# Kernel optimization log

Measured on AMD Instinct MI355X. Metric: run time of the kernel, lower is better.

Reference implementation:

```python
import jax, jax.numpy as jnp
import numpy as np

N_HEADS = 16
THETA = 10000.0


def _rope_cos_sin(seq_len, head_dim):
    # freqs_cis = exp(i * pos * theta^(-2j/d)), shape (seq_len, head_dim//2)
    inv_freq = 1.0 / (THETA ** (np.arange(0, head_dim, 2, dtype=np.float32) / head_dim))
    ang = np.arange(seq_len, dtype=np.float32)[:, None] * inv_freq[None, :]
    return jnp.asarray(np.cos(ang)), jnp.asarray(np.sin(ang))


def _apply_rope(t, cos, sin):
    # t: [B, S, H, hd]; rotate consecutive pairs as complex numbers
    B, S, H, hd = t.shape
    pairs = t.reshape(B, S, H, hd // 2, 2)
    r, i = pairs[..., 0], pairs[..., 1]
    c = cos[None, :, None, :]  # [1, S, 1, hd//2]
    s = sin[None, :, None, :]
    out_r = r * c - i * s
    out_i = r * s + i * c
    return jnp.stack([out_r, out_i], axis=-1).reshape(B, S, H, hd)


def setup_inputs() -> dict:
    key = jax.random.key(0)
    ks = jax.random.split(key, 5)
    B, S, D = 2, 2048, 2048
    scale = 1.0 / np.sqrt(D)
    return {
        "x": jax.random.normal(ks[0], (B, S, D), dtype=jnp.float32),
        "wq": jax.random.normal(ks[1], (D, D), dtype=jnp.float32) * scale,
        "wk": jax.random.normal(ks[2], (D, D), dtype=jnp.float32) * scale,
        "wv": jax.random.normal(ks[3], (D, D), dtype=jnp.float32) * scale,
        "wo": jax.random.normal(ks[4], (D, D), dtype=jnp.float32) * scale,
    }


def reference(x, wq, wk, wv, wo):
    B, S, D = x.shape
    H = N_HEADS
    hd = D // H
    cos, sin = _rope_cos_sin(S, hd)

    xq = (x @ wq.T).reshape(B, S, H, hd)
    xk = (x @ wk.T).reshape(B, S, H, hd)
    xv = (x @ wv.T).reshape(B, S, H, hd)

    xq = _apply_rope(xq, cos, sin)
    xk = _apply_rope(xk, cos, sin)

    # [B, H, S, S] scores, full (non-causal) softmax as in the source
    scores = jnp.einsum("bqhd,bkhd->bhqk", xq, xk) / jnp.sqrt(jnp.float32(hd))
    attn = jax.nn.softmax(scores, axis=-1)
    out = jnp.einsum("bhqk,bkhd->bqhd", attn, xv).reshape(B, S, D)
    return out @ wo.T
```

## Files before the change

### kernel.cpp

```cpp
#include <hip/hip_runtime.h>
#include <hip/hip_bf16.h>
#include <stdint.h>


typedef __attribute__((ext_vector_type(4))) float f32x4;
typedef __attribute__((ext_vector_type(8))) short bf16x8;

typedef __attribute__((address_space(3))) unsigned int lds_u32;
typedef __attribute__((address_space(1))) const unsigned int gbl_u32;

__device__ __forceinline__ void async16(const void* g, void* l) {
  __builtin_amdgcn_global_load_lds((gbl_u32*)g, (lds_u32*)l, 16, 0, 0);
}

__device__ __forceinline__ float bf_to_f(unsigned short u) {
  union { unsigned int i; float f; } v; v.i = ((unsigned int)u) << 16; return v.f;
}
__device__ __forceinline__ unsigned short f_to_bf(float f) {
  union { float f; unsigned int i; } v; v.f = f;
  unsigned int r = v.i + 0x7FFFu + ((v.i >> 16) & 1u);
  return (unsigned short)(r >> 16);
}
__device__ __forceinline__ unsigned int cvt_pk_bf16(float lo, float hi) {
  unsigned int r;
  asm("v_cvt_pk_bf16_f32 %0, %1, %2" : "=v"(r) : "v"(lo), "v"(hi));
  return r;
}

#define B_ 2
#define S_ 2048
#define D_ 2048
#define H_ 16
#define HD_ 128
#define KVB 128

__global__ __launch_bounds__(256) void conv_all(const float* __restrict__ x,
                                                const float* __restrict__ wq,
                                                const float* __restrict__ wk,
                                                const float* __restrict__ wv,
                                                const float* __restrict__ wo,
                                                unsigned short* __restrict__ xb,
                                                unsigned short* __restrict__ wb) {
  int i = blockIdx.x * 256 + threadIdx.x;
  const float* s;
  unsigned short* d;
  int off;
  if (i < 2097152) {
    s = x; d = xb; off = i;
  } else {
    int j = i - 2097152;
    int t = j >> 20;
    off = j & 1048575;
    s = (t == 0) ? wq : (t == 1) ? wk : (t == 2) ? wv : wo;
    d = wb + (size_t)t * 4194304;
  }
  float4 v = ((const float4*)s)[off];
  uint2 o;
  o.x = (unsigned int)f_to_bf(v.x) | ((unsigned int)f_to_bf(v.y) << 16);
  o.y = (unsigned int)f_to_bf(v.z) | ((unsigned int)f_to_bf(v.w) << 16);
  ((uint2*)d)[off] = o;
}

__global__ __launch_bounds__(256) void rope_table_kernel(float* __restrict__ cosT,
                                                         float* __restrict__ sinT) {
  int i = blockIdx.x * 256 + threadIdx.x;
  int s = i >> 6, j = i & 63;
  float inv = powf(10000.0f, -(float)(2 * j) * (1.0f / 128.0f));
  float ang = (float)s * inv;
  float sv, cv;
  sincosf(ang, &sv, &cv);
  cosT[i] = cv;
  sinT[i] = sv;
}

__global__ __launch_bounds__(256, 3) void qkv_gemm(const unsigned short* __restrict__ A,
                                                   const unsigned short* __restrict__ W,
                                                   unsigned short* __restrict__ Qb,
                                                   unsigned short* __restrict__ Kb,
                                                   unsigned short* __restrict__ Vtb,
                                                   const float* __restrict__ cosT,
                                                   const float* __restrict__ sinT) {
  __shared__ unsigned short sA[128 * 64];
  __shared__ unsigned short sB[128 * 64];
  const int K = 2048, N = 2048;
  const int tid = threadIdx.x;
  const int l = tid & 63, wv = tid >> 6;
  const int lane15 = l & 15, lhi = l >> 4;
  const int wm = wv >> 1, wn = wv & 1;
  const int bm = blockIdx.x, bn = blockIdx.y;
  const int sector = bn >> 4, bnl = bn & 15;
  const unsigned short* Ag = A + (size_t)bm * 128 * K;
  const unsigned short* Bg = W + (size_t)bn * 128 * K;

  f32x4 acc[4][4];
  const f32x4 zero = {0.f, 0.f, 0.f, 0.f};
#pragma unroll
  for (int i = 0; i < 4; i++)
#pragma unroll
    for (int j = 0; j < 4; j++) acc[i][j] = zero;

  for (int k0 = 0; k0 < K; k0 += 64) {
    __syncthreads();
#pragma unroll
    for (int i = 0; i < 4; i++) {
      int c = i * 256 + tid;
      int row = c >> 3;
      int colD = (c & 7) << 4;
      int colS = colD ^ ((row & 7) << 4);
      async16(Ag + (size_t)row * K + k0 + (colS >> 1), (char*)sA + row * 128 + colD);
      async16(Bg + (size_t)row * K + k0 + (colS >> 1), (char*)sB + row * 128 + colD);
    }
    __syncthreads();

#pragma unroll
    for (int h = 0; h < 2; h++) {
      bf16x8 af[4], bfr[4];
#pragma unroll
      for (int i = 0; i < 4; i++) {
        int row = wm * 64 + i * 16 + lane15;
        af[i] = *(const bf16x8*)((char*)sA + row * 128 +
                                 ((h * 64 + lhi * 16) ^ ((row & 7) << 4)));
      }
#pragma unroll
      for (int j = 0; j < 4; j++) {
        int row = wn * 64 + j * 16 + lane15;
        bfr[j] = *(const bf16x8*)((char*)sB + row * 128 +
                                  ((h * 64 + lhi * 16) ^ ((row & 7) << 4)));
      }
#pragma unroll
      for (int i = 0; i < 4; i++)
#pragma unroll
        for (int j = 0; j < 4; j++)
          acc[i][j] = __builtin_amdgcn_mfma_f32_16x16x32_bf16(af[i], bfr[j], acc[i][j], 0, 0, 0);
    }
  }

#pragma unroll
  for (int i = 0; i < 4; i++) {
    int m0 = bm * 128 + wm * 64 + i * 16 + lhi * 4;
#pragma unroll
    for (int j = 0; j < 4; j++) {
      int n = bnl * 128 + wn * 64 + j * 16 + lane15;
      if (sector == 0) {
#pragma unroll
        for (int r = 0; r < 4; r++) Qb[(size_t)(m0 + r) * N + n] = f_to_bf(acc[i][j][r]);
      } else if (sector == 1) {
        int s0 = m0 & (S_ - 1);
        int jp = (n & (HD_ - 1)) >> 1;
        int odd = n & 1;
#pragma unroll
        for (int r = 0; r < 4; r++) {
          float own = acc[i][j][r];
          float prt = __shfl_xor(own, 1);
          float c = cosT[(s0 + r) * 64 + jp];
          float sn = sinT[(s0 + r) * 64 + jp];
          float outv = odd ? fmaf(prt, sn, own * c) : own * c - prt * sn;
          Kb[(size_t)(m0 + r) * N + n] = f_to_bf(outv);
        }
      } else {
        int s0 = m0 & (S_ - 1);
        size_t row = (size_t)((m0 >> 11) * D_ + n);
        uint2 st;
        st.x = (unsigned int)f_to_bf(acc[i][j][0]) | ((unsigned int)f_to_bf(acc[i][j][1]) << 16);
        st.y = (unsigned int)f_to_bf(acc[i][j][2]) | ((unsigned int)f_to_bf(acc[i][j][3]) << 16);
        *(uint2*)(Vtb + row * S_ + s0) = st;
      }
    }
  }
}

__global__ __launch_bounds__(256, 3) void gemm_out(const unsigned short* __restrict__ A,
                                                   const unsigned short* __restrict__ Bm,
                                                   float* __restrict__ Cf) {
  __shared__ unsigned short sA[128 * 64];
  __shared__ unsigned short sB[128 * 64];
  const int K = 2048, N = 2048;
  const int tid = threadIdx.x;
  const int l = tid & 63, wv = tid >> 6;
  const int lane15 = l & 15, lhi = l >> 4;
  const int wm = wv >> 1, wn = wv & 1;
  const int bm = blockIdx.x, bn = blockIdx.y;
  const unsigned short* Ag = A + (size_t)bm * 128 * K;
  const unsigned short* Bg = Bm + (size_t)bn * 128 * K;

  f32x4 acc[4][4];
  const f32x4 zero = {0.f, 0.f, 0.f, 0.f};
#pragma unroll
  for (int i = 0; i < 4; i++)
#pragma unroll
    for (int j = 0; j < 4; j++) acc[i][j] = zero;

  for (int k0 = 0; k0 < K; k0 += 64) {
    __syncthreads();
#pragma unroll
    for (int i = 0; i < 4; i++) {
      int c = i * 256 + tid;
      int row = c >> 3;
      int colD = (c & 7) << 4;
      int colS = colD ^ ((row & 7) << 4);
      async16(Ag + (size_t)row * K + k0 + (colS >> 1), (char*)sA + row * 128 + colD);
      async16(Bg + (size_t)row * K + k0 + (colS >> 1), (char*)sB + row * 128 + colD);
    }
    __syncthreads();

#pragma unroll
    for (int h = 0; h < 2; h++) {
      bf16x8 af[4], bfr[4];
#pragma unroll
      for (int i = 0; i < 4; i++) {
        int row = wm * 64 + i * 16 + lane15;
        af[i] = *(const bf16x8*)((char*)sA + row * 128 +
                                 ((h * 64 + lhi * 16) ^ ((row & 7) << 4)));
      }
#pragma unroll
      for (int j = 0; j < 4; j++) {
        int row = wn * 64 + j * 16 + lane15;
        bfr[j] = *(const bf16x8*)((char*)sB + row * 128 +
                                  ((h * 64 + lhi * 16) ^ ((row & 7) << 4)));
      }
#pragma unroll
      for (int i = 0; i < 4; i++)
#pragma unroll
        for (int j = 0; j < 4; j++)
          acc[i][j] = __builtin_amdgcn_mfma_f32_16x16x32_bf16(af[i], bfr[j], acc[i][j], 0, 0, 0);
    }
  }

#pragma unroll
  for (int i = 0; i < 4; i++) {
    int m0 = bm * 128 + wm * 64 + i * 16 + lhi * 4;
#pragma unroll
    for (int j = 0; j < 4; j++) {
      int n = bn * 128 + wn * 64 + j * 16 + lane15;
#pragma unroll
      for (int r = 0; r < 4; r++) Cf[(size_t)(m0 + r) * N + n] = acc[i][j][r];
    }
  }
}

__global__ __launch_bounds__(512, 2) void attn_kernel(const unsigned short* __restrict__ Q,
                                                      const unsigned short* __restrict__ K,
                                                      const unsigned short* __restrict__ Vt,
                                                      unsigned short* __restrict__ ctx,
                                                      const float* __restrict__ cosT,
                                                      const float* __restrict__ sinT) {
  __shared__ unsigned short sK[2][KVB * 128];
  __shared__ unsigned short sV[2][128 * KVB];
  const int tid = threadIdx.x, l = tid & 63, w = tid >> 6;
  const int lane15 = l & 15, lhi = l >> 4;
  const int bh = blockIdx.x * 4 + (blockIdx.y >> 3);
  const int qt = blockIdx.y & 7;
  const int b = bh >> 4, h = bh & 15;
  const int q0 = qt * 256;
  const unsigned short* Kg = K + ((size_t)(b * S_)) * D_ + h * HD_;
  const unsigned short* Vg = Vt + ((size_t)bh * HD_) * S_;
  const float qscale = 0.08838834764831845f * 1.44269504f;
  const float THR = 11.5415603f;

  const unsigned short* gp[8];
  unsigned int lofs[8];
  size_t gstep;
  if (w < 4) {
#pragma unroll
    for (int i = 0; i < 8; i++) {
      int row = w * 32 + i * 4 + (l >> 4);
      int colD = (l & 15) << 4;
      int colS = colD ^ ((row & 7) << 4);
      gp[i] = Kg + (size_t)row * D_ + (colS >> 1);
      lofs[i] = row * 256 + colD;
    }
    gstep = (size_t)KVB * D_;
  } else {
#pragma unroll
    for (int i = 0; i < 8; i++) {
      int row = (w - 4) * 32 + i * 4 + (l >> 4);
      int colD = (l & 15) << 4;
      int colS = colD ^ ((row & 7) << 4);
      gp[i] = Vg + (size_t)row * S_ + (colS >> 1);
      lofs[i] = row * 256 + colD;
    }
    gstep = KVB;
  }

  bf16x8 qf[2][4];
#pragma unroll
  for (int s = 0; s < 2; s++) {
    int s_q = q0 + w * 32 + s * 16 + lane15;
    const unsigned short* Qrow = Q + ((size_t)(b * S_ + s_q)) * D_ + h * HD_;
#pragma unroll
    for (int kc = 0; kc < 4; kc++) {
      int d0 = kc * 32 + lhi * 8;
      uint4 raw = *(const uint4*)(Qrow + d0);
      float4 cv = *(const float4*)(cosT + (size_t)s_q * 64 + (d0 >> 1));
      float4 sv = *(const float4*)(sinT + (size_t)s_q * 64 + (d0 >> 1));
      unsigned int u[4] = {raw.x, raw.y, raw.z, raw.w};
      float cc[4] = {cv.x, cv.y, cv.z, cv.w};
      float ss[4] = {sv.x, sv.y, sv.z, sv.w};
      unsigned int o[4];
#pragma unroll
      for (int p = 0; p < 4; p++) {
        float re = bf_to_f((unsigned short)(u[p] & 0xffffu));
        float im = bf_to_f((unsigned short)(u[p] >> 16));
        float orr = (re * cc[p] - im * ss[p]) * qscale;
        float oi = (re * ss[p] + im * cc[p]) * qscale;
        o[p] = (unsigned int)f_to_bf(orr) | ((unsigned int)f_to_bf(oi) << 16);
      }
      union { uint4 u4; bf16x8 v; } cvt;
      cvt.u4.x = o[0]; cvt.u4.y = o[1]; cvt.u4.z = o[2]; cvt.u4.w = o[3];
      qf[s][kc] = cvt.v;
    }
  }

  float mrun[2] = {-1e30f, -1e30f}, lrun[2] = {0.f, 0.f};
  const f32x4 zero = {0.f, 0.f, 0.f, 0.f};
  f32x4 oacc[2][8];
#pragma unroll
  for (int s = 0; s < 2; s++)
#pragma unroll
    for (int nf = 0; nf < 8; nf++) oacc[s][nf] = zero;

  {
    char* base = (w < 4) ? (char*)&sK[0][0] : (char*)&sV[0][0];
#pragma unroll
    for (int i = 0; i < 8; i++) { async16(gp[i], base + lofs[i]); gp[i] += gstep; }
  }

  for (int t = 0; t < S_ / KVB; ++t) {
    const int cur = t & 1;
    __syncthreads();
    if (t < S_ / KVB - 1) {
      char* base = (w < 4) ? (char*)&sK[cur ^ 1][0] : (char*)&sV[cur ^ 1][0];
#pragma unroll
      for (int i = 0; i < 8; i++) { async16(gp[i], base + lofs[i]); gp[i] += gstep; }
    }
    const unsigned short* sKc = sK[cur];
    const unsigned short* sVc = sV[cur];

    f32x4 sacc[2][8];
#pragma unroll
    for (int s = 0; s < 2; s++)
#pragma unroll
      for (int n = 0; n < 8; n++) sacc[s][n] = zero;
    __builtin_amdgcn_s_setprio(1);
#pragma unroll
    for (int n = 0; n < 8; n++) {
      int row = n * 16 + lane15;
#pragma unroll
      for (int kc = 0; kc < 4; kc++) {
        bf16x8 kf = *(const bf16x8*)((const char*)sKc + row * 256 +
                                     ((kc * 64 + lhi * 16) ^ ((row & 7) << 4)));
        sacc[0][n] = __builtin_amdgcn_mfma_f32_16x16x32_bf16(kf, qf[0][kc], sacc[0][n], 0, 0, 0);
        sacc[1][n] = __builtin_amdgcn_mfma_f32_16x16x32_bf16(kf, qf[1][kc], sacc[1][n], 0, 0, 0);
      }
    }
    __builtin_amdgcn_s_setprio(0);

    float pmax[2];
#pragma unroll
    for (int s = 0; s < 2; s++) {
      float mn[8];
#pragma unroll
      for (int n = 0; n < 8; n++)
        mn[n] = fmaxf(fmaxf(sacc[s][n][0], sacc[s][n][1]), fmaxf(sacc[s][n][2], sacc[s][n][3]));
      float pm = fmaxf(fmaxf(fmaxf(mn[0], mn[1]), fmaxf(mn[2], mn[3])),
                       fmaxf(fmaxf(mn[4], mn[5]), fmaxf(mn[6], mn[7])));
      pm = fmaxf(pm, __shfl_xor(pm, 16));
      pm = fmaxf(pm, __shfl_xor(pm, 32));
      pmax[s] = pm;
    }
    if (!__all(fmaxf(pmax[0] - mrun[0], pmax[1] - mrun[1]) <= THR)) {
#pragma unroll
      for (int s = 0; s < 2; s++) {
        float mnew = fmaxf(mrun[s], pmax[s]);
        float alpha = exp2f(mrun[s] - mnew);
        lrun[s] *= alpha;
        float af[4];
#pragma unroll
        for (int r = 0; r < 4; r++) af[r] = __shfl(alpha, lhi * 4 + r);
#pragma unroll
        for (int nf = 0; nf < 8; nf++)
#pragma unroll
          for (int r = 0; r < 4; r++) oacc[s][nf][r] *= af[r];
        mrun[s] = mnew;
      }
    }
    bf16x8 paS[2][4];
#pragma unroll
    for (int s = 0; s < 2; s++) {
      float rs = 0.f;
      unsigned int wlo[8], whi[8];
#pragma unroll
      for (int n = 0; n < 8; n++) {
        float p0 = exp2f(sacc[s][n][0] - mrun[s]);
        float p1 = exp2f(sacc[s][n][1] - mrun[s]);
        float p2 = exp2f(sacc[s][n][2] - mrun[s]);
        float p3 = exp2f(sacc[s][n][3] - mrun[s]);
        rs += (p0 + p1) + (p2 + p3);
        wlo[n] = cvt_pk_bf16(p0, p1);
        whi[n] = cvt_pk_bf16(p2, p3);
      }
      rs += __shfl_xor(rs, 16);
      rs += __shfl_xor(rs, 32);
      lrun[s] += rs;
#pragma unroll
      for (int kc = 0; kc < 4; kc++) {
        unsigned int A = wlo[2 * kc], Bw = whi[2 * kc];
        unsigned int C = wlo[2 * kc + 1], Dw = whi[2 * kc + 1];
        asm("v_permlane32_swap_b32 %0, %1" : "+v"(A), "+v"(C));
        asm("v_permlane16_swap_b32 %0, %1" : "+v"(A), "+v"(C));
        asm("v_permlane32_swap_b32 %0, %1" : "+v"(Bw), "+v"(Dw));
        asm("v_permlane16_swap_b32 %0, %1" : "+v"(Bw), "+v"(Dw));
        union { uint4 u4; bf16x8 v; } pk;
        pk.u4.x = A; pk.u4.y = Bw; pk.u4.z = C; pk.u4.w = Dw;
        paS[s][kc] = pk.v;
      }
    }

    __builtin_amdgcn_s_setprio(1);
#pragma unroll
    for (int nf = 0; nf < 8; nf++) {
      int row = nf * 16 + lane15;
#pragma unroll
      for (int kc = 0; kc < 4; kc++) {
        bf16x8 vf = *(const bf16x8*)((const char*)sVc + row * 256 +
                                     ((kc * 64 + lhi * 16) ^ ((row & 7) << 4)));
        oacc[0][nf] = __builtin_amdgcn_mfma_f32_16x16x32_bf16(paS[0][kc], vf, oacc[0][nf], 0, 0, 0);
        oacc[1][nf] = __builtin_amdgcn_mfma_f32_16x16x32_bf16(paS[1][kc], vf, oacc[1][nf], 0, 0, 0);
      }
    }
    __builtin_amdgcn_s_setprio(0);
  }

#pragma unroll
  for (int s = 0; s < 2; s++) {
    float inv = 1.0f / lrun[s];
    float invr[4];
#pragma unroll
    for (int r = 0; r < 4; r++) invr[r] = __shfl(inv, lhi * 4 + r);
    unsigned short* Og = ctx + ((size_t)(b * S_ + q0 + w * 32 + s * 16)) * D_ + h * HD_;
#pragma unroll
    for (int r = 0; r < 4; r++) {
      int qrow = lhi * 4 + r;
#pragma unroll
      for (int nf = 0; nf < 8; nf++)
        Og[(size_t)qrow * D_ + nf * 16 + lane15] = f_to_bf(oacc[s][nf][r] * invr[r]);
    }
  }
}

extern "C" void kernel_launch(void* const* d_in, const int* in_sizes, int n_in,
                              void* d_out, int out_size, void* d_ws, size_t ws_size,
                              hipStream_t stream) {
  (void)in_sizes; (void)n_in; (void)out_size; (void)ws_size;
  const float* x = (const float*)d_in[0];
  const float* wq = (const float*)d_in[1];
  const float* wk = (const float*)d_in[2];
  const float* wv = (const float*)d_in[3];
  const float* wo = (const float*)d_in[4];
  float* out = (float*)d_out;

  char* ws = (char*)d_ws;
  const size_t MB = 1024 * 1024;
  unsigned short* xb  = (unsigned short*)(ws + 0 * MB);
  unsigned short* wqb = (unsigned short*)(ws + 16 * MB);
  unsigned short* wob = (unsigned short*)(ws + 40 * MB);
  unsigned short* Qb  = (unsigned short*)(ws + 48 * MB);
  unsigned short* Kb  = (unsigned short*)(ws + 64 * MB);
  unsigned short* Vtb = (unsigned short*)(ws + 80 * MB);
  float* cosT = (float*)(ws + 96 * MB);
  float* sinT = (float*)(ws + 96 * MB + 524288);
  unsigned short* ctxb = xb;

  const int M = B_ * S_;

  conv_all<<<24576, 256, 0, stream>>>(x, wq, wk, wv, wo, xb, wqb);
  rope_table_kernel<<<512, 256, 0, stream>>>(cosT, sinT);

  qkv_gemm<<<dim3(M / 128, 48), 256, 0, stream>>>(xb, wqb, Qb, Kb, Vtb, cosT, sinT);

  attn_kernel<<<dim3(8, 32), 512, 0, stream>>>(Qb, Kb, Vtb, ctxb, cosT, sinT);

  gemm_out<<<dim3(M / 128, D_ / 128), 256, 0, stream>>>(ctxb, wob, out);
}
```

Measured before the change: 272.0 us.

## Double-buffer LDS tiles in QKV and output GEMMs with MFMA priority boost

Both GEMM kernels now keep two LDS stages for the A and B tiles. The next K-slice is prefetched with async global-to-LDS loads while MFMAs run on the current slice, and each iteration needs one barrier instead of two. Source pointers and LDS offsets are precomputed and advanced each step. s_setprio is raised around the MFMA block. The cost is twice the LDS per block, so launch bounds drop from 3 to 2 blocks per CU, which lowers occupancy in exchange for overlapping load latency with compute.

```diff
diff --git a/kernel.cpp b/kernel.cpp
--- a/kernel.cpp
+++ b/kernel.cpp
@@ -73,15 +73,15 @@
   sinT[i] = sv;
 }
 
-__global__ __launch_bounds__(256, 3) void qkv_gemm(const unsigned short* __restrict__ A,
+__global__ __launch_bounds__(256, 2) void qkv_gemm(const unsigned short* __restrict__ A,
                                                    const unsigned short* __restrict__ W,
                                                    unsigned short* __restrict__ Qb,
                                                    unsigned short* __restrict__ Kb,
                                                    unsigned short* __restrict__ Vtb,
                                                    const float* __restrict__ cosT,
                                                    const float* __restrict__ sinT) {
-  __shared__ unsigned short sA[128 * 64];
-  __shared__ unsigned short sB[128 * 64];
+  __shared__ unsigned short sA[2][128 * 64];
+  __shared__ unsigned short sB[2][128 * 64];
   const int K = 2048, N = 2048;
   const int tid = threadIdx.x;
   const int l = tid & 63, wv = tid >> 6;
@@ -89,8 +89,20 @@
   const int wm = wv >> 1, wn = wv & 1;
   const int bm = blockIdx.x, bn = blockIdx.y;
   const int sector = bn >> 4, bnl = bn & 15;
-  const unsigned short* Ag = A + (size_t)bm * 128 * K;
-  const unsigned short* Bg = W + (size_t)bn * 128 * K;
+
+  const int srow = tid >> 3;
+  const int colD = (tid & 7) << 4;
+  const unsigned short* aSrc[4];
+  const unsigned short* bSrc[4];
+  unsigned int lofs[4];
+#pragma unroll
+  for (int i = 0; i < 4; i++) {
+    int row = i * 32 + srow;
+    int cS = colD ^ ((row & 7) << 4);
+    aSrc[i] = A + (size_t)(bm * 128 + row) * K + (cS >> 1);
+    bSrc[i] = W + (size_t)(bn * 128 + row) * K + (cS >> 1);
+    lofs[i] = row * 128 + colD;
+  }
 
   f32x4 acc[4][4];
   const f32x4 zero = {0.f, 0.f, 0.f, 0.f};
@@ -99,18 +111,24 @@
 #pragma unroll
     for (int j = 0; j < 4; j++) acc[i][j] = zero;
 
-  for (int k0 = 0; k0 < K; k0 += 64) {
+#pragma unroll
+  for (int i = 0; i < 4; i++) {
+    async16(aSrc[i], (char*)&sA[0][0] + lofs[i]); aSrc[i] += 64;
+    async16(bSrc[i], (char*)&sB[0][0] + lofs[i]); bSrc[i] += 64;
+  }
+
+  for (int t = 0; t < 32; ++t) {
+    const int cur = t & 1;
     __syncthreads();
-#pragma unroll
-    for (int i = 0; i < 4; i++) {
-      int c = i * 256 + tid;
-      int row = c >> 3;
-      int colD = (c & 7) << 4;
-      int colS = colD ^ ((row & 7) << 4);
-      async16(Ag + (size_t)row * K + k0 + (colS >> 1), (char*)sA + row * 128 + colD);
-      async16(Bg + (size_t)row * K + k0 + (colS >> 1), (char*)sB + row * 128 + colD);
-    }
-    __syncthreads();
+    if (t < 31) {
+#pragma unroll
+      for (int i = 0; i < 4; i++) {
+        async16(aSrc[i], (char*)&sA[cur ^ 1][0] + lofs[i]); aSrc[i] += 64;
+        async16(bSrc[i], (char*)&sB[cur ^ 1][0] + lofs[i]); bSrc[i] += 64;
+      }
+    }
+    const char* sAc = (const char*)&sA[cur][0];
+    const char* sBc = (const char*)&sB[cur][0];
 
 #pragma unroll
     for (int h = 0; h < 2; h++) {
@@ -118,20 +136,22 @@
 #pragma unroll
       for (int i = 0; i < 4; i++) {
         int row = wm * 64 + i * 16 + lane15;
-        af[i] = *(const bf16x8*)((char*)sA + row * 128 +
+        af[i] = *(const bf16x8*)(sAc + row * 128 +
                                  ((h * 64 + lhi * 16) ^ ((row & 7) << 4)));
       }
 #pragma unroll
       for (int j = 0; j < 4; j++) {
         int row = wn * 64 + j * 16 + lane15;
-        bfr[j] = *(const bf16x8*)((char*)sB + row * 128 +
+        bfr[j] = *(const bf16x8*)(sBc + row * 128 +
                                   ((h * 64 + lhi * 16) ^ ((row & 7) << 4)));
       }
+      __builtin_amdgcn_s_setprio(1);
 #pragma unroll
       for (int i = 0; i < 4; i++)
 #pragma unroll
         for (int j = 0; j < 4; j++)
           acc[i][j] = __builtin_amdgcn_mfma_f32_16x16x32_bf16(af[i], bfr[j], acc[i][j], 0, 0, 0);
+      __builtin_amdgcn_s_setprio(0);
     }
   }
 
@@ -169,19 +189,31 @@
   }
 }
 
-__global__ __launch_bounds__(256, 3) void gemm_out(const unsigned short* __restrict__ A,
+__global__ __launch_bounds__(256, 2) void gemm_out(const unsigned short* __restrict__ A,
                                                    const unsigned short* __restrict__ Bm,
                                                    float* __restrict__ Cf) {
-  __shared__ unsigned short sA[128 * 64];
-  __shared__ unsigned short sB[128 * 64];
+  __shared__ unsigned short sA[2][128 * 64];
+  __shared__ unsigned short sB[2][128 * 64];
   const int K = 2048, N = 2048;
   const int tid = threadIdx.x;
   const int l = tid & 63, wv = tid >> 6;
   const int lane15 = l & 15, lhi = l >> 4;
   const int wm = wv >> 1, wn = wv & 1;
   const int bm = blockIdx.x, bn = blockIdx.y;
-  const unsigned short* Ag = A + (size_t)bm * 128 * K;
-  const unsigned short* Bg = Bm + (size_t)bn * 128 * K;
+
+  const int srow = tid >> 3;
+  const int colD = (tid & 7) << 4;
+  const unsigned short* aSrc[4];
+  const unsigned short* bSrc[4];
+  unsigned int lofs[4];
+#pragma unroll
+  for (int i = 0; i < 4; i++) {
+    int row = i * 32 + srow;
+    int cS = colD ^ ((row & 7) << 4);
+    aSrc[i] = A + (size_t)(bm * 128 + row) * K + (cS >> 1);
+    bSrc[i] = Bm + (size_t)(bn * 128 + row) * K + (cS >> 1);
+    lofs[i] = row * 128 + colD;
+  }
 
   f32x4 acc[4][4];
   const f32x4 zero = {0.f, 0.f, 0.f, 0.f};
@@ -190,18 +222,24 @@
 #pragma unroll
     for (int j = 0; j < 4; j++) acc[i][j] = zero;
 
-  for (int k0 = 0; k0 < K; k0 += 64) {
+#pragma unroll
+  for (int i = 0; i < 4; i++) {
+    async16(aSrc[i], (char*)&sA[0][0] + lofs[i]); aSrc[i] += 64;
+    async16(bSrc[i], (char*)&sB[0][0] + lofs[i]); bSrc[i] += 64;
+  }
+
+  for (int t = 0; t < 32; ++t) {
+    const int cur = t & 1;
     __syncthreads();
-#pragma unroll
-    for (int i = 0; i < 4; i++) {
-      int c = i * 256 + tid;
-      int row = c >> 3;
-      int colD = (c & 7) << 4;
-      int colS = colD ^ ((row & 7) << 4);
-      async16(Ag + (size_t)row * K + k0 + (colS >> 1), (char*)sA + row * 128 + colD);
-      async16(Bg + (size_t)row * K + k0 + (colS >> 1), (char*)sB + row * 128 + colD);
-    }
-    __syncthreads();
+    if (t < 31) {
+#pragma unroll
+      for (int i = 0; i < 4; i++) {
+        async16(aSrc[i], (char*)&sA[cur ^ 1][0] + lofs[i]); aSrc[i] += 64;
+        async16(bSrc[i], (char*)&sB[cur ^ 1][0] + lofs[i]); bSrc[i] += 64;
+      }
+    }
+    const char* sAc = (const char*)&sA[cur][0];
+    const char* sBc = (const char*)&sB[cur][0];
 
 #pragma unroll
     for (int h = 0; h < 2; h++) {
@@ -209,20 +247,22 @@
 #pragma unroll
       for (int i = 0; i < 4; i++) {
         int row = wm * 64 + i * 16 + lane15;
-        af[i] = *(const bf16x8*)((char*)sA + row * 128 +
+        af[i] = *(const bf16x8*)(sAc + row * 128 +
                                  ((h * 64 + lhi * 16) ^ ((row & 7) << 4)));
       }
 #pragma unroll
       for (int j = 0; j < 4; j++) {
         int row = wn * 64 + j * 16 + lane15;
-        bfr[j] = *(const bf16x8*)((char*)sB + row * 128 +
+        bfr[j] = *(const bf16x8*)(sBc + row * 128 +
                                   ((h * 64 + lhi * 16) ^ ((row & 7) << 4)));
       }
+      __builtin_amdgcn_s_setprio(1);
 #pragma unroll
       for (int i = 0; i < 4; i++)
 #pragma unroll
         for (int j = 0; j < 4; j++)
           acc[i][j] = __builtin_amdgcn_mfma_f32_16x16x32_bf16(af[i], bfr[j], acc[i][j], 0, 0, 0);
+      __builtin_amdgcn_s_setprio(0);
     }
   }
 
```

Result: no change. 267.5 us (-1.7%).

## Double-buffer LDS tiles in QKV and output GEMMs with async prefetch

Applied to the files above, without the earlier changes.

Both projection GEMMs now split each K step into 32-wide tiles held in two LDS buffers. The async global-to-LDS load for the next tile is issued right after the single barrier, so it overlaps the MFMA work on the current tile. This removes the old second barrier per step, which stalled on load completion before any compute could start. Source pointers and LDS offsets are precomputed with a new swizzle, and s_setprio raises wave priority around the MFMA block. In exchange there are twice as many loop iterations and barriers per K, and a smaller tile per step.

```diff
diff --git a/kernel.cpp b/kernel.cpp
--- a/kernel.cpp
+++ b/kernel.cpp
@@ -80,8 +80,8 @@
                                                    unsigned short* __restrict__ Vtb,
                                                    const float* __restrict__ cosT,
                                                    const float* __restrict__ sinT) {
-  __shared__ unsigned short sA[128 * 64];
-  __shared__ unsigned short sB[128 * 64];
+  __shared__ unsigned short sA[2][128 * 32];
+  __shared__ unsigned short sB[2][128 * 32];
   const int K = 2048, N = 2048;
   const int tid = threadIdx.x;
   const int l = tid & 63, wv = tid >> 6;
@@ -89,8 +89,20 @@
   const int wm = wv >> 1, wn = wv & 1;
   const int bm = blockIdx.x, bn = blockIdx.y;
   const int sector = bn >> 4, bnl = bn & 15;
-  const unsigned short* Ag = A + (size_t)bm * 128 * K;
-  const unsigned short* Bg = W + (size_t)bn * 128 * K;
+
+  const unsigned short* aSrc[2];
+  const unsigned short* bSrc[2];
+  unsigned int lofs[2];
+#pragma unroll
+  for (int i = 0; i < 2; i++) {
+    int c = i * 256 + tid;
+    int row = c >> 2;
+    int colD = (c & 3) << 4;
+    int colS = colD ^ (((row >> 1) & 3) << 4);
+    aSrc[i] = A + (size_t)(bm * 128 + row) * K + (colS >> 1);
+    bSrc[i] = W + (size_t)(bn * 128 + row) * K + (colS >> 1);
+    lofs[i] = row * 64 + colD;
+  }
 
   f32x4 acc[4][4];
   const f32x4 zero = {0.f, 0.f, 0.f, 0.f};
@@ -99,40 +111,45 @@
 #pragma unroll
     for (int j = 0; j < 4; j++) acc[i][j] = zero;
 
-  for (int k0 = 0; k0 < K; k0 += 64) {
+#pragma unroll
+  for (int i = 0; i < 2; i++) {
+    async16(aSrc[i], (char*)&sA[0][0] + lofs[i]); aSrc[i] += 32;
+    async16(bSrc[i], (char*)&sB[0][0] + lofs[i]); bSrc[i] += 32;
+  }
+
+  for (int t = 0; t < 64; ++t) {
+    const int cur = t & 1;
     __syncthreads();
+    if (t < 63) {
+#pragma unroll
+      for (int i = 0; i < 2; i++) {
+        async16(aSrc[i], (char*)&sA[cur ^ 1][0] + lofs[i]); aSrc[i] += 32;
+        async16(bSrc[i], (char*)&sB[cur ^ 1][0] + lofs[i]); bSrc[i] += 32;
+      }
+    }
+    const char* sAc = (const char*)&sA[cur][0];
+    const char* sBc = (const char*)&sB[cur][0];
+
+    bf16x8 af[4], bfr[4];
 #pragma unroll
     for (int i = 0; i < 4; i++) {
-      int c = i * 256 + tid;
-      int row = c >> 3;
-      int colD = (c & 7) << 4;
-      int colS = colD ^ ((row & 7) << 4);
-      async16(Ag + (size_t)row * K + k0 + (colS >> 1), (char*)sA + row * 128 + colD);
-      async16(Bg + (size_t)row * K + k0 + (colS >> 1), (char*)sB + row * 128 + colD);
-    }
-    __syncthreads();
-
-#pragma unroll
-    for (int h = 0; h < 2; h++) {
-      bf16x8 af[4], bfr[4];
-#pragma unroll
-      for (int i = 0; i < 4; i++) {
-        int row = wm * 64 + i * 16 + lane15;
-        af[i] = *(const bf16x8*)((char*)sA + row * 128 +
-                                 ((h * 64 + lhi * 16) ^ ((row & 7) << 4)));
-      }
-#pragma unroll
-      for (int j = 0; j < 4; j++) {
-        int row = wn * 64 + j * 16 + lane15;
-        bfr[j] = *(const bf16x8*)((char*)sB + row * 128 +
-                                  ((h * 64 + lhi * 16) ^ ((row & 7) << 4)));
-      }
-#pragma unroll
-      for (int i = 0; i < 4; i++)
-#pragma unroll
-        for (int j = 0; j < 4; j++)
-          acc[i][j] = __builtin_amdgcn_mfma_f32_16x16x32_bf16(af[i], bfr[j], acc[i][j], 0, 0, 0);
-    }
+      int row = wm * 64 + i * 16 + lane15;
+      af[i] = *(const bf16x8*)(sAc + row * 64 +
+                               ((lhi * 16) ^ (((row >> 1) & 3) << 4)));
+    }
+#pragma unroll
+    for (int j = 0; j < 4; j++) {
+      int row = wn * 64 + j * 16 + lane15;
+      bfr[j] = *(const bf16x8*)(sBc + row * 64 +
+                                ((lhi * 16) ^ (((row >> 1) & 3) << 4)));
+    }
+    __builtin_amdgcn_s_setprio(1);
+#pragma unroll
+    for (int i = 0; i < 4; i++)
+#pragma unroll
+      for (int j = 0; j < 4; j++)
+        acc[i][j] = __builtin_amdgcn_mfma_f32_16x16x32_bf16(af[i], bfr[j], acc[i][j], 0, 0, 0);
+    __builtin_amdgcn_s_setprio(0);
   }
 
 #pragma unroll
@@ -172,16 +189,28 @@
 __global__ __launch_bounds__(256, 3) void gemm_out(const unsigned short* __restrict__ A,
                                                    const unsigned short* __restrict__ Bm,
                                                    float* __restrict__ Cf) {
-  __shared__ unsigned short sA[128 * 64];
-  __shared__ unsigned short sB[128 * 64];
+  __shared__ unsigned short sA[2][128 * 32];
+  __shared__ unsigned short sB[2][128 * 32];
   const int K = 2048, N = 2048;
   const int tid = threadIdx.x;
   const int l = tid & 63, wv = tid >> 6;
   const int lane15 = l & 15, lhi = l >> 4;
   const int wm = wv >> 1, wn = wv & 1;
   const int bm = blockIdx.x, bn = blockIdx.y;
-  const unsigned short* Ag = A + (size_t)bm * 128 * K;
-  const unsigned short* Bg = Bm + (size_t)bn * 128 * K;
+
+  const unsigned short* aSrc[2];
+  const unsigned short* bSrc[2];
+  unsigned int lofs[2];
+#pragma unroll
+  for (int i = 0; i < 2; i++) {
+    int c = i * 256 + tid;
+    int row = c >> 2;
+    int colD = (c & 3) << 4;
+    int colS = colD ^ (((row >> 1) & 3) << 4);
+    aSrc[i] = A + (size_t)(bm * 128 + row) * K + (colS >> 1);
+    bSrc[i] = Bm + (size_t)(bn * 128 + row) * K + (colS >> 1);
+    lofs[i] = row * 64 + colD;
+  }
 
   f32x4 acc[4][4];
   const f32x4 zero = {0.f, 0.f, 0.f, 0.f};
@@ -190,40 +219,45 @@
 #pragma unroll
     for (int j = 0; j < 4; j++) acc[i][j] = zero;
 
-  for (int k0 = 0; k0 < K; k0 += 64) {
+#pragma unroll
+  for (int i = 0; i < 2; i++) {
+    async16(aSrc[i], (char*)&sA[0][0] + lofs[i]); aSrc[i] += 32;
+    async16(bSrc[i], (char*)&sB[0][0] + lofs[i]); bSrc[i] += 32;
+  }
+
+  for (int t = 0; t < 64; ++t) {
+    const int cur = t & 1;
     __syncthreads();
+    if (t < 63) {
+#pragma unroll
+      for (int i = 0; i < 2; i++) {
+        async16(aSrc[i], (char*)&sA[cur ^ 1][0] + lofs[i]); aSrc[i] += 32;
+        async16(bSrc[i], (char*)&sB[cur ^ 1][0] + lofs[i]); bSrc[i] += 32;
+      }
+    }
+    const char* sAc = (const char*)&sA[cur][0];
+    const char* sBc = (const char*)&sB[cur][0];
+
+    bf16x8 af[4], bfr[4];
 #pragma unroll
     for (int i = 0; i < 4; i++) {
-      int c = i * 256 + tid;
-      int row = c >> 3;
-      int colD = (c & 7) << 4;
-      int colS = colD ^ ((row & 7) << 4);
-      async16(Ag + (size_t)row * K + k0 + (colS >> 1), (char*)sA + row * 128 + colD);
-      async16(Bg + (size_t)row * K + k0 + (colS >> 1), (char*)sB + row * 128 + colD);
-    }
-    __syncthreads();
-
-#pragma unroll
-    for (int h = 0; h < 2; h++) {
-      bf16x8 af[4], bfr[4];
-#pragma unroll
-      for (int i = 0; i < 4; i++) {
-        int row = wm * 64 + i * 16 + lane15;
-        af[i] = *(const bf16x8*)((char*)sA + row * 128 +
-                                 ((h * 64 + lhi * 16) ^ ((row & 7) << 4)));
-      }
-#pragma unroll
-      for (int j = 0; j < 4; j++) {
-        int row = wn * 64 + j * 16 + lane15;
-        bfr[j] = *(const bf16x8*)((char*)sB + row * 128 +
-                                  ((h * 64 + lhi * 16) ^ ((row & 7) << 4)));
-      }
-#pragma unroll
-      for (int i = 0; i < 4; i++)
-#pragma unroll
-        for (int j = 0; j < 4; j++)
-          acc[i][j] = __builtin_amdgcn_mfma_f32_16x16x32_bf16(af[i], bfr[j], acc[i][j], 0, 0, 0);
-    }
+      int row = wm * 64 + i * 16 + lane15;
+      af[i] = *(const bf16x8*)(sAc + row * 64 +
+                               ((lhi * 16) ^ (((row >> 1) & 3) << 4)));
+    }
+#pragma unroll
+    for (int j = 0; j < 4; j++) {
+      int row = wn * 64 + j * 16 + lane15;
+      bfr[j] = *(const bf16x8*)(sBc + row * 64 +
+                                ((lhi * 16) ^ (((row >> 1) & 3) << 4)));
+    }
+    __builtin_amdgcn_s_setprio(1);
+#pragma unroll
+    for (int i = 0; i < 4; i++)
+#pragma unroll
+      for (int j = 0; j < 4; j++)
+        acc[i][j] = __builtin_amdgcn_mfma_f32_16x16x32_bf16(af[i], bfr[j], acc[i][j], 0, 0, 0);
+    __builtin_amdgcn_s_setprio(0);
   }
 
 #pragma unroll
```

Result: slower. 288.1 us (+5.9%).
